# Kernel optimization log

Hardware: AMD Instinct MI355X
Metric: run time of the kernel (lower is better)

The kernel has to match this reference:

```python
import jax, jax.numpy as jnp
import numpy as np

N_NODES = 50000
N_EDGES = 800000
IN_CH = 128
HID = 64
N_GRAPHS = 512


def setup_inputs() -> dict:
    key = jax.random.key(0)
    ks = jax.random.split(key, 16)
    s = 0.05
    x = jax.random.normal(ks[0], (N_NODES, IN_CH), dtype=jnp.float32)
    edge_index = jax.random.randint(ks[1], (2, N_EDGES), 0, N_NODES, dtype=jnp.int32)
    batch = jnp.sort(jax.random.randint(ks[2], (N_NODES,), 0, N_GRAPHS, dtype=jnp.int32))
    return {
        "x": x,
        "edge_index": edge_index,
        "batch": batch,
        # GraphConv layer 1: lin_rel (weight+bias) applied to aggregated neighbors, lin_root (no bias)
        "W_rel1": jax.random.normal(ks[3], (IN_CH, HID), dtype=jnp.float32) * s,
        "b_rel1": jnp.zeros((HID,), dtype=jnp.float32),
        "W_root1": jax.random.normal(ks[4], (IN_CH, HID), dtype=jnp.float32) * s,
        "W_rel2": jax.random.normal(ks[5], (HID, HID), dtype=jnp.float32) * s,
        "b_rel2": jnp.zeros((HID,), dtype=jnp.float32),
        "W_root2": jax.random.normal(ks[6], (HID, HID), dtype=jnp.float32) * s,
        "W_rel3": jax.random.normal(ks[7], (HID, HID), dtype=jnp.float32) * s,
        "b_rel3": jnp.zeros((HID,), dtype=jnp.float32),
        "W_root3": jax.random.normal(ks[8], (HID, HID), dtype=jnp.float32) * s,
        "W_fc1": jax.random.normal(ks[9], (HID, 32), dtype=jnp.float32) * s,
        "b_fc1": jnp.zeros((32,), dtype=jnp.float32),
        "W_fc2": jax.random.normal(ks[10], (32, 1), dtype=jnp.float32) * s,
        "b_fc2": jnp.zeros((1,), dtype=jnp.float32),
    }


def reference(x, edge_index, batch,
              W_rel1, b_rel1, W_root1,
              W_rel2, b_rel2, W_root2,
              W_rel3, b_rel3, W_root3,
              W_fc1, b_fc1, W_fc2, b_fc2):
    src, dst = edge_index[0], edge_index[1]  # messages flow src -> dst

    def graph_conv(h, W_rel, b_rel, W_root):
        # PyG GraphConv: out = lin_rel(sum_{j in N(i)} h_j) + lin_root(h_i)
        agg = jax.ops.segment_sum(h[src], dst, num_segments=N_NODES)  # [N, d]
        return agg @ W_rel + b_rel + h @ W_root

    h = jax.nn.relu(graph_conv(x, W_rel1, b_rel1, W_root1))
    h = jax.nn.relu(graph_conv(h, W_rel2, b_rel2, W_root2))
    h = jax.nn.relu(graph_conv(h, W_rel3, b_rel3, W_root3))

    # global_mean_pool over graphs in the batch
    sums = jax.ops.segment_sum(h, batch, num_segments=N_GRAPHS)          # [G, 64]
    cnts = jax.ops.segment_sum(jnp.ones((h.shape[0], 1), h.dtype), batch,
                               num_segments=N_GRAPHS)                     # [G, 1]
    pooled = sums / jnp.maximum(cnts, 1.0)

    out = jax.nn.relu(pooled @ W_fc1 + b_fc1)
    return (out @ W_fc2 + b_fc2).reshape(-1)  # [G]
```

## Files before the change

### kernel.cpp

```cpp
#include <hip/hip_runtime.h>
#include <cstdint>
#include <cstddef>

#define NN 50000
#define NE 800000
#define GRAPHS 512
#define NBK 782
#define CAP 2048
#define GG1 782

typedef __attribute__((ext_vector_type(8))) short bf16x8;
typedef __attribute__((ext_vector_type(4))) float f32x4;
typedef __attribute__((ext_vector_type(2))) float f32x2;

__device__ __forceinline__ unsigned short f2bf(float f) {
  union { float f; unsigned u; } v; v.f = f;
  unsigned r = v.u + 0x7FFF + ((v.u >> 16) & 1);
  return (unsigned short)(r >> 16);
}
__device__ __forceinline__ float bf2f(unsigned short h) {
  union { unsigned u; float f; } v; v.u = ((unsigned)h) << 16;
  return v.f;
}

__device__ __forceinline__ unsigned char f2fp8_sw(float f) {
  union { float f; unsigned u; } v; v.f = f;
  unsigned s = (v.u >> 24) & 0x80;
  unsigned u = v.u & 0x7fffffffu;
  if (u < 0x3c000000u) {
    float a = fabsf(f) * 512.0f;
    int mi = (int)(a + 0.5f); if (mi > 7) mi = 7;
    return (unsigned char)(s | mi);
  }
  unsigned r = u + 0x7FFFF + ((u >> 20) & 1);
  int e = (int)(r >> 23) - 127;
  unsigned m = (r >> 20) & 7;
  if (e > 8) { e = 8; m = 6; }
  return (unsigned char)(s | ((unsigned)(e + 7) << 3) | m);
}
__device__ __forceinline__ float fp82f_sw(unsigned b) {
  unsigned s = (b & 0x80) << 24;
  unsigned e = (b >> 3) & 0xF, m = b & 7;
  union { unsigned u; float f; } v;
  if (e == 0) {
    float sub = (float)m * 0.001953125f;
    return (b & 0x80) ? -sub : sub;
  }
  v.u = s | ((e + 120) << 23) | (m << 20);
  return v.f;
}
__device__ __forceinline__ void fp8pair(float a, float b,
                                        unsigned char& c0, unsigned char& c1) {
#if __has_builtin(__builtin_amdgcn_cvt_pk_fp8_f32)
  int p = __builtin_amdgcn_cvt_pk_fp8_f32(a, b, 0, false);
  c0 = (unsigned char)(p & 0xFF); c1 = (unsigned char)((p >> 8) & 0xFF);
#else
  c0 = f2fp8_sw(a); c1 = f2fp8_sw(b);
#endif
}
__device__ __forceinline__ float4 fp8x4_dec(unsigned u) {
#if __has_builtin(__builtin_amdgcn_cvt_pk_f32_fp8)
  f32x2 lo = __builtin_amdgcn_cvt_pk_f32_fp8((int)u, false);
  f32x2 hi = __builtin_amdgcn_cvt_pk_f32_fp8((int)u, true);
  return make_float4(lo[0], lo[1], hi[0], hi[1]);
#else
  return make_float4(fp82f_sw(u & 0xFF), fp82f_sw((u >> 8) & 0xFF),
                     fp82f_sw((u >> 16) & 0xFF), fp82f_sw((u >> 24) & 0xFF));
#endif
}

__global__ __launch_bounds__(256) void setup_kernel(
    const int* __restrict__ batch, int* __restrict__ gstart,
    int* __restrict__ bcnt, float* __restrict__ pooled,
    const float* __restrict__ Wrel1, const float* __restrict__ Wroot1,
    const float* __restrict__ Wrel2, const float* __restrict__ Wroot2,
    const float* __restrict__ Wrel3, const float* __restrict__ Wroot3,
    unsigned short* __restrict__ Wt1, unsigned short* __restrict__ Wt2,
    unsigned short* __restrict__ Wt3) {
  const int tid = blockIdx.x * 256 + threadIdx.x;
  const int stride = gridDim.x * 256;
  for (int i = tid; i < NBK; i += stride) bcnt[i] = 0;
  for (int i = tid; i < GRAPHS * 64; i += stride) pooled[i] = 0.f;
  for (int g = tid; g <= GRAPHS; g += stride) {
    int lo = 0, hi = NN;
    while (lo < hi) {
      int mid = (lo + hi) >> 1;
      if (batch[mid] < g) lo = mid + 1; else hi = mid;
    }
    gstart[g] = lo;
  }
  for (int idx = tid; idx < 128 * 128; idx += stride) {
    int c = idx >> 7, k = idx & 127;
    Wt1[c * 128 + k] = f2bf(c < 64 ? Wrel1[k * 64 + c] : Wroot1[k * 64 + (c - 64)]);
  }
  for (int idx = tid; idx < 128 * 64; idx += stride) {
    int c = idx >> 6, k = idx & 63;
    Wt2[c * 64 + k] = f2bf(c < 64 ? Wrel2[k * 64 + c] : Wroot2[k * 64 + (c - 64)]);
    Wt3[c * 64 + k] = f2bf(c < 64 ? Wrel3[k * 64 + c] : Wroot3[k * 64 + (c - 64)]);
  }
}

__global__ __launch_bounds__(256) void bin_gemm1_kernel(
    const float* __restrict__ h, const unsigned short* __restrict__ Wt,
    const float* __restrict__ brel,
    unsigned char* __restrict__ hW, unsigned short* __restrict__ root,
    const int* __restrict__ src, const int* __restrict__ dst,
    int* __restrict__ bcnt, unsigned* __restrict__ ebuf) {
  __shared__ __align__(16) char smem[49152];
  const int t = threadIdx.x;

  if (blockIdx.x < GG1) {
    constexpr int K = 128;
    unsigned short* as = (unsigned short*)smem;
    unsigned short* bs = (unsigned short*)(smem + 16384);
    constexpr int SEG = K / 8;
    const int row0 = blockIdx.x * 64;

    for (int idx = t; idx < 64 * SEG; idx += 256) {
      int r = idx / SEG, kq = idx % SEG;
      int node = row0 + r;
      float4 v0 = make_float4(0.f, 0.f, 0.f, 0.f), v1 = v0;
      if (node < NN) {
        const float* p = &h[(size_t)node * K + kq * 8];
        v0 = *(const float4*)p; v1 = *(const float4*)(p + 4);
      }
      uint4 p;
      p.x = f2bf(v0.x) | ((unsigned)f2bf(v0.y) << 16);
      p.y = f2bf(v0.z) | ((unsigned)f2bf(v0.w) << 16);
      p.z = f2bf(v1.x) | ((unsigned)f2bf(v1.y) << 16);
      p.w = f2bf(v1.z) | ((unsigned)f2bf(v1.w) << 16);
      int sidx = (r * K + kq * 8) ^ ((r & 7) << 3);
      *(uint4*)&as[sidx] = p;
    }
    for (int idx = t; idx < 128 * SEG; idx += 256) {
      int c = idx / SEG, kq = idx % SEG;
      uint4 v = *(const uint4*)&Wt[c * K + kq * 8];
      int sidx = (c * K + kq * 8) ^ ((c & 7) << 3);
      *(uint4*)&bs[sidx] = v;
    }
    __syncthreads();

    const int lane = t & 63, wave = t >> 6;
    const int li = lane & 15;
    const int kg = (lane >> 4) * 8;
    const int ar = wave * 16 + li;
    f32x4 acc[8];
    #pragma unroll
    for (int i = 0; i < 8; ++i) acc[i] = (f32x4){0.f, 0.f, 0.f, 0.f};

    #pragma unroll
    for (int k0 = 0; k0 < K; k0 += 32) {
      int ka = k0 + kg;
      bf16x8 a = *(bf16x8*)&as[(ar * K + ka) ^ ((ar & 7) << 3)];
      #pragma unroll
      for (int nb = 0; nb < 8; ++nb) {
        int bc = nb * 16 + li;
        bf16x8 b = *(bf16x8*)&bs[(bc * K + ka) ^ ((bc & 7) << 3)];
        acc[nb] = __builtin_amdgcn_mfma_f32_16x16x32_bf16(a, b, acc[nb], 0, 0, 0);
      }
    }

    const int orow = row0 + wave * 16 + (lane >> 4) * 4;
    #pragma unroll
    for (int nb = 0; nb < 4; ++nb) {
      unsigned char cb[4];
      fp8pair(acc[nb][0], acc[nb][1], cb[0], cb[1]);
      fp8pair(acc[nb][2], acc[nb][3], cb[2], cb[3]);
      #pragma unroll
      for (int r = 0; r < 4; ++r) {
        int node = orow + r;
        if (node < NN) hW[(size_t)node * 64 + nb * 16 + li] = cb[r];
      }
    }
    #pragma unroll
    for (int nb = 4; nb < 8; ++nb) {
      float bb = brel[(nb - 4) * 16 + li];
      #pragma unroll
      for (int r = 0; r < 4; ++r) {
        int node = orow + r;
        if (node < NN) root[(size_t)node * 64 + (nb - 4) * 16 + li] = f2bf(acc[nb][r] + bb);
      }
    }
  } else {
    int* hist = (int*)smem;
    int* base = hist + NBK;
    int* lcur = base + NBK;
    for (int b = t; b < NBK; b += 256) { hist[b] = 0; lcur[b] = 0; }
    __syncthreads();
    const int e0 = (blockIdx.x - GG1) * 4096;
    unsigned pk[16]; int bk[16];
    #pragma unroll
    for (int i = 0; i < 16; ++i) {
      int e = e0 + i * 256 + t;
      if (e < NE) {
        int s = src[e], d = dst[e];
        bk[i] = d >> 6;
        pk[i] = ((unsigned)(d & 63) << 17) | (unsigned)s;
        atomicAdd(&hist[bk[i]], 1);
      } else bk[i] = -1;
    }
    __syncthreads();
    for (int b = t; b < NBK; b += 256) {
      int c = hist[b];
      if (c) base[b] = atomicAdd(&bcnt[b], c);
    }
    __syncthreads();
    #pragma unroll
    for (int i = 0; i < 16; ++i) {
      if (bk[i] >= 0) {
        int r = atomicAdd(&lcur[bk[i]], 1);
        ebuf[(size_t)bk[i] * CAP + base[bk[i]] + r] = pk[i];
      }
    }
  }
}

__global__ __launch_bounds__(256) void bucket_csr_kernel(const unsigned* __restrict__ ebuf,
                                                         const int* __restrict__ bcnt,
                                                         int* __restrict__ rs,
                                                         int* __restrict__ ren,
                                                         int* __restrict__ ssrc) {
  __shared__ int ehist[64];
  __shared__ int sd[64];
  __shared__ int ecur[64];
  const int t = threadIdx.x;
  const int b = blockIdx.x;
  const int n0 = b << 6;
  const int e0 = b * CAP;
  const int cnt = bcnt[b];
  if (t < 64) ehist[t] = 0;
  __syncthreads();
  for (int e = t; e < cnt; e += 256)
    atomicAdd(&ehist[ebuf[e0 + e] >> 17], 1);
  __syncthreads();
  if (t < 64) sd[t] = ehist[t];
  __syncthreads();
  for (int off = 1; off < 64; off <<= 1) {
    int u = (t >= off && t < 64) ? sd[t - off] : 0;
    __syncthreads();
    if (t < 64) sd[t] += u;
    __syncthreads();
  }
  if (t < 64) {
    int ex = e0 + sd[t] - ehist[t];
    ecur[t] = ex;
    rs[n0 + t] = ex;
    ren[n0 + t] = e0 + sd[t];
  }
  __syncthreads();
  for (int e = t; e < cnt; e += 256) {
    unsigned ed = ebuf[e0 + e];
    int r = atomicAdd(&ecur[ed >> 17], 1);
    ssrc[r] = (int)(ed & 0x1FFFF);
  }
}

__global__ __launch_bounds__(256) void agg_gemm_kernel(
    const unsigned short* __restrict__ rootPrev,
    const unsigned char* __restrict__ hWp,
    const int* __restrict__ rs, const int* __restrict__ ren,
    const int* __restrict__ ssrc,
    const unsigned short* __restrict__ Wt,
    const float* __restrict__ brel,
    unsigned char* __restrict__ hW,
    unsigned short* __restrict__ rootOut) {
  __shared__ __align__(16) unsigned short as[16 * 64];
  __shared__ __align__(16) unsigned short bs[128 * 64];
  const int t = threadIdx.x;
  const int n0 = blockIdx.x * 16;

  #pragma unroll
  for (int i = 0; i < 4; ++i) {
    int idx = t + i * 256;
    int c = idx >> 3, kq = idx & 7;
    uint4 v = *(const uint4*)&Wt[c * 64 + kq * 8];
    int sidx = (c * 64 + kq * 8) ^ ((c & 7) << 3);
    *(uint4*)&bs[sidx] = v;
  }

  const int r = t >> 4, l16 = t & 15, c4 = l16 * 4;
  const int node = n0 + r;
  ushort4 rt = *(const ushort4*)&rootPrev[(size_t)node * 64 + c4];
  float4 a0 = make_float4(bf2f(rt.x), bf2f(rt.y), bf2f(rt.z), bf2f(rt.w));
  float4 a1 = make_float4(0.f, 0.f, 0.f, 0.f);
  const int s0 = rs[node], s1 = ren[node];
  int e = s0;
  for (; e + 2 <= s1; e += 2) {
    int sA = ssrc[e], sB = ssrc[e + 1];
    unsigned uA = *(const unsigned*)&hWp[(size_t)sA * 64 + c4];
    unsigned uB = *(const unsigned*)&hWp[(size_t)sB * 64 + c4];
    float4 vA = fp8x4_dec(uA), vB = fp8x4_dec(uB);
    a0.x += vA.x; a0.y += vA.y; a0.z += vA.z; a0.w += vA.w;
    a1.x += vB.x; a1.y += vB.y; a1.z += vB.z; a1.w += vB.w;
  }
  if (e < s1) {
    unsigned uA = *(const unsigned*)&hWp[(size_t)ssrc[e] * 64 + c4];
    float4 vA = fp8x4_dec(uA);
    a0.x += vA.x; a0.y += vA.y; a0.z += vA.z; a0.w += vA.w;
  }
  a0.x = fmaxf(a0.x + a1.x, 0.f); a0.y = fmaxf(a0.y + a1.y, 0.f);
  a0.z = fmaxf(a0.z + a1.z, 0.f); a0.w = fmaxf(a0.w + a1.w, 0.f);
  uint2 p;
  p.x = f2bf(a0.x) | ((unsigned)f2bf(a0.y) << 16);
  p.y = f2bf(a0.z) | ((unsigned)f2bf(a0.w) << 16);
  *(uint2*)&as[(r * 64 + c4) ^ ((r & 7) << 3)] = p;
  __syncthreads();

  const int lane = t & 63, wave = t >> 6;
  const int li = lane & 15, kg = (lane >> 4) * 8;
  f32x4 acc[2];
  acc[0] = (f32x4){0.f, 0.f, 0.f, 0.f};
  acc[1] = (f32x4){0.f, 0.f, 0.f, 0.f};
  #pragma unroll
  for (int ks = 0; ks < 2; ++ks) {
    int ka = ks * 32 + kg;
    bf16x8 a = *(bf16x8*)&as[(li * 64 + ka) ^ ((li & 7) << 3)];
    #pragma unroll
    for (int nb = 0; nb < 2; ++nb) {
      int bc = wave * 32 + nb * 16 + li;
      bf16x8 b = *(bf16x8*)&bs[(bc * 64 + ka) ^ ((bc & 7) << 3)];
      acc[nb] = __builtin_amdgcn_mfma_f32_16x16x32_bf16(a, b, acc[nb], 0, 0, 0);
    }
  }

  const int orow = n0 + (lane >> 4) * 4;
  if (wave < 2) {
    #pragma unroll
    for (int nb = 0; nb < 2; ++nb) {
      int col = wave * 32 + nb * 16 + li;
      unsigned char cb[4];
      fp8pair(acc[nb][0], acc[nb][1], cb[0], cb[1]);
      fp8pair(acc[nb][2], acc[nb][3], cb[2], cb[3]);
      #pragma unroll
      for (int rr = 0; rr < 4; ++rr)
        hW[(size_t)(orow + rr) * 64 + col] = cb[rr];
    }
  } else {
    #pragma unroll
    for (int nb = 0; nb < 2; ++nb) {
      int col = (wave - 2) * 32 + nb * 16 + li;
      float bb = brel[col];
      #pragma unroll
      for (int rr = 0; rr < 4; ++rr)
        rootOut[(size_t)(orow + rr) * 64 + col] = f2bf(acc[nb][rr] + bb);
    }
  }
}

__global__ __launch_bounds__(256) void agg_pool_kernel(
    const unsigned short* __restrict__ rootPrev,
    const unsigned char* __restrict__ hWp,
    const int* __restrict__ rs, const int* __restrict__ ren,
    const int* __restrict__ ssrc,
    const int* __restrict__ batch,
    float* __restrict__ pooled) {
  __shared__ float h3s[16 * 64];
  __shared__ int batch_s[16];
  const int t = threadIdx.x;
  const int n0 = blockIdx.x * 16;
  if (t < 16) batch_s[t] = batch[n0 + t];

  const int r = t >> 4, l16 = t & 15, c4 = l16 * 4;
  const int node = n0 + r;
  const int s0 = rs[node], s1 = ren[node];
  ushort4 rt = *(const ushort4*)&rootPrev[(size_t)node * 64 + c4];
  float4 a0 = make_float4(bf2f(rt.x), bf2f(rt.y), bf2f(rt.z), bf2f(rt.w));
  float4 a1 = make_float4(0.f, 0.f, 0.f, 0.f);
  int e = s0;
  for (; e + 2 <= s1; e += 2) {
    int sA = ssrc[e], sB = ssrc[e + 1];
    unsigned uA = *(const unsigned*)&hWp[(size_t)sA * 64 + c4];
    unsigned uB = *(const unsigned*)&hWp[(size_t)sB * 64 + c4];
    float4 vA = fp8x4_dec(uA), vB = fp8x4_dec(uB);
    a0.x += vA.x; a0.y += vA.y; a0.z += vA.z; a0.w += vA.w;
    a1.x += vB.x; a1.y += vB.y; a1.z += vB.z; a1.w += vB.w;
  }
  if (e < s1) {
    unsigned uA = *(const unsigned*)&hWp[(size_t)ssrc[e] * 64 + c4];
    float4 vA = fp8x4_dec(uA);
    a0.x += vA.x; a0.y += vA.y; a0.z += vA.z; a0.w += vA.w;
  }
  float4 o;
  o.x = fmaxf(a0.x + a1.x, 0.f); o.y = fmaxf(a0.y + a1.y, 0.f);
  o.z = fmaxf(a0.z + a1.z, 0.f); o.w = fmaxf(a0.w + a1.w, 0.f);
  *(float4*)&h3s[r * 64 + c4] = o;
  __syncthreads();

  if (t < 64) {
    int cur = batch_s[0]; float acc = 0.f;
    #pragma unroll
    for (int rr = 0; rr < 16; ++rr) {
      int g = batch_s[rr];
      if (g != cur) {
        unsafeAtomicAdd(&pooled[cur * 64 + t], acc);
        acc = 0.f; cur = g;
      }
      acc += h3s[rr * 64 + t];
    }
    unsafeAtomicAdd(&pooled[cur * 64 + t], acc);
  }
}

__global__ __launch_bounds__(64) void head_kernel(
    const float* __restrict__ pooled, const int* __restrict__ gstart,
    const float* __restrict__ Wfc1, const float* __restrict__ bfc1,
    const float* __restrict__ Wfc2, const float* __restrict__ bfc2,
    float* __restrict__ out) {
  __shared__ float m[64];
  __shared__ float h1[32];
  const int g = blockIdx.x, l = threadIdx.x;
  float c = fmaxf((float)(gstart[g + 1] - gstart[g]), 1.0f);
  m[l] = pooled[g * 64 + l] / c;
  __syncthreads();
  if (l < 32) {
    float a = bfc1[l];
    #pragma unroll
    for (int k = 0; k < 64; ++k) a += m[k] * Wfc1[k * 32 + l];
    h1[l] = fmaxf(a, 0.f);
  }
  __syncthreads();
  if (l == 0) {
    float o = bfc2[0];
    #pragma unroll
    for (int j = 0; j < 32; ++j) o += h1[j] * Wfc2[j];
    out[g] = o;
  }
}

extern "C" void kernel_launch(void* const* d_in, const int* in_sizes, int n_in,
                              void* d_out, int out_size, void* d_ws, size_t ws_size,
                              hipStream_t stream) {
  const float* x      = (const float*)d_in[0];
  const int*   ei     = (const int*)d_in[1];
  const int*   batch  = (const int*)d_in[2];
  const float* Wrel1  = (const float*)d_in[3];
  const float* brel1  = (const float*)d_in[4];
  const float* Wroot1 = (const float*)d_in[5];
  const float* Wrel2  = (const float*)d_in[6];
  const float* brel2  = (const float*)d_in[7];
  const float* Wroot2 = (const float*)d_in[8];
  const float* Wrel3  = (const float*)d_in[9];
  const float* brel3  = (const float*)d_in[10];
  const float* Wroot3 = (const float*)d_in[11];
  const float* Wfc1   = (const float*)d_in[12];
  const float* bfc1   = (const float*)d_in[13];
  const float* Wfc2   = (const float*)d_in[14];
  const float* bfc2   = (const float*)d_in[15];
  const int* src = ei;
  const int* dst = ei + NE;

  char* w = (char*)d_ws;
  auto alloc = [&](size_t bytes) -> char* {
    char* p = w; w += (bytes + 255) & ~(size_t)255; return p;
  };
  unsigned char*  hWa   = (unsigned char*)alloc((size_t)NN * 64);
  unsigned char*  hWb   = (unsigned char*)alloc((size_t)NN * 64);
  unsigned short* rootA = (unsigned short*)alloc((size_t)NN * 64 * 2);
  unsigned short* rootB = (unsigned short*)alloc((size_t)NN * 64 * 2);
  int*   rs     = (int*)alloc((size_t)NBK * 64 * 4);
  int*   ren    = (int*)alloc((size_t)NBK * 64 * 4);
  int*   ssrc   = (int*)alloc((size_t)NBK * CAP * 4);
  int*   gstart = (int*)alloc((size_t)(GRAPHS + 1) * 4);
  int*   bcnt   = (int*)alloc((size_t)NBK * 4);
  float* pooled = (float*)alloc((size_t)GRAPHS * 64 * 4);
  unsigned* ebuf = (unsigned*)alloc((size_t)NBK * CAP * 4);
  unsigned short* Wt1 = (unsigned short*)alloc((size_t)128 * 128 * 2);
  unsigned short* Wt2 = (unsigned short*)alloc((size_t)128 * 64 * 2);
  unsigned short* Wt3 = (unsigned short*)alloc((size_t)128 * 64 * 2);

  setup_kernel<<<64, 256, 0, stream>>>(batch, gstart, bcnt, pooled,
                                       Wrel1, Wroot1, Wrel2, Wroot2, Wrel3, Wroot3,
                                       Wt1, Wt2, Wt3);
  bin_gemm1_kernel<<<GG1 + (NE + 4095) / 4096, 256, 0, stream>>>(
      x, Wt1, brel1, hWa, rootA, src, dst, bcnt, ebuf);
  bucket_csr_kernel<<<NBK, 256, 0, stream>>>(ebuf, bcnt, rs, ren, ssrc);

  agg_gemm_kernel<<<NN / 16, 256, 0, stream>>>(rootA, hWa, rs, ren, ssrc,
                                               Wt2, brel2, hWb, rootB);
  agg_gemm_kernel<<<NN / 16, 256, 0, stream>>>(rootB, hWb, rs, ren, ssrc,
                                               Wt3, brel3, hWa, rootA);
  agg_pool_kernel<<<NN / 16, 256, 0, stream>>>(rootA, hWa, rs, ren, ssrc,
                                               batch, pooled);
  head_kernel<<<GRAPHS, 64, 0, stream>>>(pooled, gstart, Wfc1, bfc1, Wfc2, bfc2,
                                         (float*)d_out);
}
```

Baseline: 111.4 us.

## Narrow CSR source indices to 16-bit, unroll gathers, load GEMM1 A into registers

The sorted source-index array is stored as 16-bit values instead of 32-bit, which halves index traffic in every aggregation pass; node ids stay below 65536, so this is safe. The neighbor gather moves into a shared helper that is unrolled by four with four partial accumulators, to keep more independent loads in flight. The first GEMM also loads its A fragments straight from global memory into registers instead of staging them in LDS, which shrinks shared memory per block and removes one staging round-trip. In exchange, the A-operand global loads are less coalesced, and more accumulators raise register pressure.

```diff
diff --git a/kernel.cpp b/kernel.cpp
--- a/kernel.cpp
+++ b/kernel.cpp
@@ -106,57 +106,57 @@
     unsigned char* __restrict__ hW, unsigned short* __restrict__ root,
     const int* __restrict__ src, const int* __restrict__ dst,
     int* __restrict__ bcnt, unsigned* __restrict__ ebuf) {
-  __shared__ __align__(16) char smem[49152];
+  __shared__ __align__(16) char smem[32768];
   const int t = threadIdx.x;
 
   if (blockIdx.x < GG1) {
     constexpr int K = 128;
-    unsigned short* as = (unsigned short*)smem;
-    unsigned short* bs = (unsigned short*)(smem + 16384);
+    unsigned short* bs = (unsigned short*)smem;
     constexpr int SEG = K / 8;
     const int row0 = blockIdx.x * 64;
 
-    for (int idx = t; idx < 64 * SEG; idx += 256) {
-      int r = idx / SEG, kq = idx % SEG;
-      int node = row0 + r;
-      float4 v0 = make_float4(0.f, 0.f, 0.f, 0.f), v1 = v0;
-      if (node < NN) {
-        const float* p = &h[(size_t)node * K + kq * 8];
-        v0 = *(const float4*)p; v1 = *(const float4*)(p + 4);
-      }
-      uint4 p;
-      p.x = f2bf(v0.x) | ((unsigned)f2bf(v0.y) << 16);
-      p.y = f2bf(v0.z) | ((unsigned)f2bf(v0.w) << 16);
-      p.z = f2bf(v1.x) | ((unsigned)f2bf(v1.y) << 16);
-      p.w = f2bf(v1.z) | ((unsigned)f2bf(v1.w) << 16);
-      int sidx = (r * K + kq * 8) ^ ((r & 7) << 3);
-      *(uint4*)&as[sidx] = p;
-    }
     for (int idx = t; idx < 128 * SEG; idx += 256) {
       int c = idx / SEG, kq = idx % SEG;
       uint4 v = *(const uint4*)&Wt[c * K + kq * 8];
       int sidx = (c * K + kq * 8) ^ ((c & 7) << 3);
       *(uint4*)&bs[sidx] = v;
     }
-    __syncthreads();
 
     const int lane = t & 63, wave = t >> 6;
     const int li = lane & 15;
     const int kg = (lane >> 4) * 8;
-    const int ar = wave * 16 + li;
+    const int ar_node = row0 + wave * 16 + li;
+    const bool valid = ar_node < NN;
+
+    bf16x8 af[4];
+    #pragma unroll
+    for (int i = 0; i < 4; ++i) {
+      float4 v0 = make_float4(0.f, 0.f, 0.f, 0.f), v1 = v0;
+      if (valid) {
+        const float* p = &h[(size_t)ar_node * K + i * 32 + kg];
+        v0 = *(const float4*)p; v1 = *(const float4*)(p + 4);
+      }
+      union { bf16x8 b; uint4 u; } pk;
+      pk.u.x = f2bf(v0.x) | ((unsigned)f2bf(v0.y) << 16);
+      pk.u.y = f2bf(v0.z) | ((unsigned)f2bf(v0.w) << 16);
+      pk.u.z = f2bf(v1.x) | ((unsigned)f2bf(v1.y) << 16);
+      pk.u.w = f2bf(v1.z) | ((unsigned)f2bf(v1.w) << 16);
+      af[i] = pk.b;
+    }
+    __syncthreads();
+
     f32x4 acc[8];
     #pragma unroll
     for (int i = 0; i < 8; ++i) acc[i] = (f32x4){0.f, 0.f, 0.f, 0.f};
 
     #pragma unroll
-    for (int k0 = 0; k0 < K; k0 += 32) {
-      int ka = k0 + kg;
-      bf16x8 a = *(bf16x8*)&as[(ar * K + ka) ^ ((ar & 7) << 3)];
+    for (int i = 0; i < 4; ++i) {
+      int ka = i * 32 + kg;
       #pragma unroll
       for (int nb = 0; nb < 8; ++nb) {
         int bc = nb * 16 + li;
         bf16x8 b = *(bf16x8*)&bs[(bc * K + ka) ^ ((bc & 7) << 3)];
-        acc[nb] = __builtin_amdgcn_mfma_f32_16x16x32_bf16(a, b, acc[nb], 0, 0, 0);
+        acc[nb] = __builtin_amdgcn_mfma_f32_16x16x32_bf16(af[i], b, acc[nb], 0, 0, 0);
       }
     }
 
@@ -219,7 +219,7 @@
                                                          const int* __restrict__ bcnt,
                                                          int* __restrict__ rs,
                                                          int* __restrict__ ren,
-                                                         int* __restrict__ ssrc) {
+                                                         unsigned short* __restrict__ ssrc) {
   __shared__ int ehist[64];
   __shared__ int sd[64];
   __shared__ int ecur[64];
@@ -251,15 +251,48 @@
   for (int e = t; e < cnt; e += 256) {
     unsigned ed = ebuf[e0 + e];
     int r = atomicAdd(&ecur[ed >> 17], 1);
-    ssrc[r] = (int)(ed & 0x1FFFF);
-  }
+    ssrc[r] = (unsigned short)(ed & 0xFFFF);
+  }
+}
+
+__device__ __forceinline__ float4 gather_node(
+    const unsigned short* __restrict__ rootPrev,
+    const unsigned char* __restrict__ hWp,
+    const unsigned short* __restrict__ ssrc,
+    int node, int c4, int s0, int s1) {
+  ushort4 rt = *(const ushort4*)&rootPrev[(size_t)node * 64 + c4];
+  float4 a0 = make_float4(bf2f(rt.x), bf2f(rt.y), bf2f(rt.z), bf2f(rt.w));
+  float4 a1 = make_float4(0.f, 0.f, 0.f, 0.f);
+  float4 a2 = make_float4(0.f, 0.f, 0.f, 0.f);
+  float4 a3 = make_float4(0.f, 0.f, 0.f, 0.f);
+  int e = s0;
+  for (; e + 4 <= s1; e += 4) {
+    unsigned uA = *(const unsigned*)&hWp[(size_t)ssrc[e] * 64 + c4];
+    unsigned uB = *(const unsigned*)&hWp[(size_t)ssrc[e + 1] * 64 + c4];
+    unsigned uC = *(const unsigned*)&hWp[(size_t)ssrc[e + 2] * 64 + c4];
+    unsigned uD = *(const unsigned*)&hWp[(size_t)ssrc[e + 3] * 64 + c4];
+    float4 vA = fp8x4_dec(uA), vB = fp8x4_dec(uB);
+    float4 vC = fp8x4_dec(uC), vD = fp8x4_dec(uD);
+    a0.x += vA.x; a0.y += vA.y; a0.z += vA.z; a0.w += vA.w;
+    a1.x += vB.x; a1.y += vB.y; a1.z += vB.z; a1.w += vB.w;
+    a2.x += vC.x; a2.y += vC.y; a2.z += vC.z; a2.w += vC.w;
+    a3.x += vD.x; a3.y += vD.y; a3.z += vD.z; a3.w += vD.w;
+  }
+  for (; e < s1; ++e) {
+    unsigned uA = *(const unsigned*)&hWp[(size_t)ssrc[e] * 64 + c4];
+    float4 vA = fp8x4_dec(uA);
+    a0.x += vA.x; a0.y += vA.y; a0.z += vA.z; a0.w += vA.w;
+  }
+  a0.x += a1.x + a2.x + a3.x; a0.y += a1.y + a2.y + a3.y;
+  a0.z += a1.z + a2.z + a3.z; a0.w += a1.w + a2.w + a3.w;
+  return a0;
 }
 
 __global__ __launch_bounds__(256) void agg_gemm_kernel(
     const unsigned short* __restrict__ rootPrev,
     const unsigned char* __restrict__ hWp,
     const int* __restrict__ rs, const int* __restrict__ ren,
-    const int* __restrict__ ssrc,
+    const unsigned short* __restrict__ ssrc,
     const unsigned short* __restrict__ Wt,
     const float* __restrict__ brel,
     unsigned char* __restrict__ hW,
@@ -280,26 +313,9 @@
 
   const int r = t >> 4, l16 = t & 15, c4 = l16 * 4;
   const int node = n0 + r;
-  ushort4 rt = *(const ushort4*)&rootPrev[(size_t)node * 64 + c4];
-  float4 a0 = make_float4(bf2f(rt.x), bf2f(rt.y), bf2f(rt.z), bf2f(rt.w));
-  float4 a1 = make_float4(0.f, 0.f, 0.f, 0.f);
-  const int s0 = rs[node], s1 = ren[node];
-  int e = s0;
-  for (; e + 2 <= s1; e += 2) {
-    int sA = ssrc[e], sB = ssrc[e + 1];
-    unsigned uA = *(const unsigned*)&hWp[(size_t)sA * 64 + c4];
-    unsigned uB = *(const unsigned*)&hWp[(size_t)sB * 64 + c4];
-    float4 vA = fp8x4_dec(uA), vB = fp8x4_dec(uB);
-    a0.x += vA.x; a0.y += vA.y; a0.z += vA.z; a0.w += vA.w;
-    a1.x += vB.x; a1.y += vB.y; a1.z += vB.z; a1.w += vB.w;
-  }
-  if (e < s1) {
-    unsigned uA = *(const unsigned*)&hWp[(size_t)ssrc[e] * 64 + c4];
-    float4 vA = fp8x4_dec(uA);
-    a0.x += vA.x; a0.y += vA.y; a0.z += vA.z; a0.w += vA.w;
-  }
-  a0.x = fmaxf(a0.x + a1.x, 0.f); a0.y = fmaxf(a0.y + a1.y, 0.f);
-  a0.z = fmaxf(a0.z + a1.z, 0.f); a0.w = fmaxf(a0.w + a1.w, 0.f);
+  float4 a0 = gather_node(rootPrev, hWp, ssrc, node, c4, rs[node], ren[node]);
+  a0.x = fmaxf(a0.x, 0.f); a0.y = fmaxf(a0.y, 0.f);
+  a0.z = fmaxf(a0.z, 0.f); a0.w = fmaxf(a0.w, 0.f);
   uint2 p;
   p.x = f2bf(a0.x) | ((unsigned)f2bf(a0.y) << 16);
   p.y = f2bf(a0.z) | ((unsigned)f2bf(a0.w) << 16);
@@ -351,7 +367,7 @@
     const unsigned short* __restrict__ rootPrev,
     const unsigned char* __restrict__ hWp,
     const int* __restrict__ rs, const int* __restrict__ ren,
-    const int* __restrict__ ssrc,
+    const unsigned short* __restrict__ ssrc,
     const int* __restrict__ batch,
     float* __restrict__ pooled) {
   __shared__ float h3s[16 * 64];
@@ -362,27 +378,10 @@
 
   const int r = t >> 4, l16 = t & 15, c4 = l16 * 4;
   const int node = n0 + r;
-  const int s0 = rs[node], s1 = ren[node];
-  ushort4 rt = *(const ushort4*)&rootPrev[(size_t)node * 64 + c4];
-  float4 a0 = make_float4(bf2f(rt.x), bf2f(rt.y), bf2f(rt.z), bf2f(rt.w));
-  float4 a1 = make_float4(0.f, 0.f, 0.f, 0.f);
-  int e = s0;
-  for (; e + 2 <= s1; e += 2) {
-    int sA = ssrc[e], sB = ssrc[e + 1];
-    unsigned uA = *(const unsigned*)&hWp[(size_t)sA * 64 + c4];
-    unsigned uB = *(const unsigned*)&hWp[(size_t)sB * 64 + c4];
-    float4 vA = fp8x4_dec(uA), vB = fp8x4_dec(uB);
-    a0.x += vA.x; a0.y += vA.y; a0.z += vA.z; a0.w += vA.w;
-    a1.x += vB.x; a1.y += vB.y; a1.z += vB.z; a1.w += vB.w;
-  }
-  if (e < s1) {
-    unsigned uA = *(const unsigned*)&hWp[(size_t)ssrc[e] * 64 + c4];
-    float4 vA = fp8x4_dec(uA);
-    a0.x += vA.x; a0.y += vA.y; a0.z += vA.z; a0.w += vA.w;
-  }
+  float4 a0 = gather_node(rootPrev, hWp, ssrc, node, c4, rs[node], ren[node]);
   float4 o;
-  o.x = fmaxf(a0.x + a1.x, 0.f); o.y = fmaxf(a0.y + a1.y, 0.f);
-  o.z = fmaxf(a0.z + a1.z, 0.f); o.w = fmaxf(a0.w + a1.w, 0.f);
+  o.x = fmaxf(a0.x, 0.f); o.y = fmaxf(a0.y, 0.f);
+  o.z = fmaxf(a0.z, 0.f); o.w = fmaxf(a0.w, 0.f);
   *(float4*)&h3s[r * 64 + c4] = o;
   __syncthreads();
 
@@ -459,7 +458,7 @@
   unsigned short* rootB = (unsigned short*)alloc((size_t)NN * 64 * 2);
   int*   rs     = (int*)alloc((size_t)NBK * 64 * 4);
   int*   ren    = (int*)alloc((size_t)NBK * 64 * 4);
-  int*   ssrc   = (int*)alloc((size_t)NBK * CAP * 4);
+  unsigned short* ssrc = (unsigned short*)alloc((size_t)NBK * CAP * 2);
   int*   gstart = (int*)alloc((size_t)(GRAPHS + 1) * 4);
   int*   bcnt   = (int*)alloc((size_t)NBK * 4);
   float* pooled = (float*)alloc((size_t)GRAPHS * 64 * 4);
```

New measurement: 91.59 us. 17.8% less time.
